# Optimization experiments

Measured on AMD Instinct MI355X. Metric: run time of the kernel, lower is better.

## Reference

```python
import jax, jax.numpy as jnp
import numpy as np

D_MODEL = 1024
H = 16
D_K = D_MODEL // H
B = 2
S = 2048


def setup_inputs() -> dict:
    key = jax.random.key(0)
    ks = jax.random.split(key, 11)
    scale = 1.0 / np.sqrt(D_MODEL)
    inp = {
        "query": jax.random.normal(ks[0], (B, S, D_MODEL), jnp.float32),
        "key_in": jax.random.normal(ks[1], (B, S, D_MODEL), jnp.float32),
        "value": jax.random.normal(ks[2], (B, S, D_MODEL), jnp.float32),
        # causal mask, broadcast over heads: 1 = keep, 0 = masked
        "mask": jnp.tril(jnp.ones((S, S), jnp.int32))[None, None, :, :].repeat(B, axis=0),
        "w_q": jax.random.normal(ks[3], (D_MODEL, D_MODEL), jnp.float32) * scale,
        "b_q": jax.random.normal(ks[4], (D_MODEL,), jnp.float32) * 0.01,
        "w_k": jax.random.normal(ks[5], (D_MODEL, D_MODEL), jnp.float32) * scale,
        "b_k": jax.random.normal(ks[6], (D_MODEL,), jnp.float32) * 0.01,
        "w_v": jax.random.normal(ks[7], (D_MODEL, D_MODEL), jnp.float32) * scale,
        "b_v": jax.random.normal(ks[8], (D_MODEL,), jnp.float32) * 0.01,
        "w_out": jax.random.normal(ks[9], (D_MODEL, D_MODEL), jnp.float32) * scale,
        "b_out": jax.random.normal(ks[10], (D_MODEL,), jnp.float32) * 0.01,
    }
    return inp


def _split_heads(x):
    # [B,S,D] -> [B,H,S,d_k]
    b, s, _ = x.shape
    return x.reshape(b, s, H, D_K).transpose(0, 2, 1, 3)


def reference(query, key_in, value, mask, w_q, b_q, w_k, b_k, w_v, b_v, w_out, b_out):
    q = _split_heads(query @ w_q.T + b_q)
    k = _split_heads(key_in @ w_k.T + b_k)
    v = _split_heads(value @ w_v.T + b_v)
    scores = jnp.einsum("bhqd,bhkd->bhqk", q, k) / jnp.sqrt(jnp.float32(D_K))
    scores = jnp.where(mask == 0, jnp.float32(-1e9), scores)
    attn = jax.nn.softmax(scores, axis=-1)  # dropout rate 0.0 -> identity
    out = jnp.einsum("bhqk,bhkd->bhqd", attn, v)
    out = out.transpose(0, 2, 1, 3).reshape(query.shape[0], -1, D_MODEL)
    return out @ w_out.T + b_out
```

## Files before the change

kernel.cpp:

```cpp
#include <hip/hip_runtime.h>
#include <hip/hip_bf16.h>

#define D_MODEL 1024
#define NH 16
#define DKH 64
#define BB 2
#define SS 2048
#define MTOT (BB * SS)

typedef __hip_bfloat16 bf16;
typedef __attribute__((ext_vector_type(8))) short short8;
typedef __attribute__((ext_vector_type(4))) short short4v;
typedef __attribute__((ext_vector_type(4))) float floatx4;

__device__ __forceinline__ bf16 f2bf(float x) { return __float2bfloat16(x); }

__device__ __forceinline__ void async_cp16(const void* g, void* l) {
  __builtin_amdgcn_global_load_lds(
      (const __attribute__((address_space(1))) unsigned int*)g,
      (__attribute__((address_space(3))) unsigned int*)l, 16, 0, 0);
}

__global__ __launch_bounds__(256) void convert_kernel(
    const float* __restrict__ wq, const float* __restrict__ wk,
    const float* __restrict__ wv, const float* __restrict__ wo,
    const float* __restrict__ qi, const float* __restrict__ ki,
    const float* __restrict__ vi, bf16* __restrict__ Wb,
    bf16* __restrict__ Qi, bf16* __restrict__ Ki, bf16* __restrict__ Vi) {
  const int id = blockIdx.x * 256 + threadIdx.x;
  const float* src;
  bf16* dst;
  if (id < (1 << 20)) {
    const int m = id >> 18, loc = id & 0x3FFFF;
    src = ((m == 0) ? wq : (m == 1) ? wk : (m == 2) ? wv : wo) + (size_t)loc * 4;
    dst = Wb + ((size_t)m << 20) + (size_t)loc * 4;
  } else {
    const int t = id - (1 << 20);
    const int m = t >> 20, loc = t & 0xFFFFF;
    src = ((m == 0) ? qi : (m == 1) ? ki : vi) + (size_t)loc * 4;
    dst = ((m == 0) ? Qi : (m == 1) ? Ki : Vi) + (size_t)loc * 4;
  }
  const float4 v = *(const float4*)src;
  short4v s;
  bf16* pb = (bf16*)&s;
  pb[0] = f2bf(v.x); pb[1] = f2bf(v.y); pb[2] = f2bf(v.z); pb[3] = f2bf(v.w);
  *(short4v*)dst = s;
}

__device__ __forceinline__ void gemm_qkv_body(const bf16* __restrict__ A,
                                              const bf16* __restrict__ W,
                                              const float* __restrict__ Bi,
                                              bf16* __restrict__ C, int mode) {
  constexpr int N = 1024, K = 1024;
  __shared__ bf16 As[2][128 * 32];
  __shared__ bf16 Ws[2][128 * 32];

  const int tid = threadIdx.x;
  const int w = tid >> 6, lane = tid & 63, quad = lane >> 4, n16 = lane & 15;
  const int bx = blockIdx.x;
  const int bm = bx & 31, bn = bx >> 5;
  const int wm = (w & 1) * 64, wn = (w >> 1) * 64;

  const int rb = lane >> 2, cb = lane & 3;

  const bf16* Ag0 = A + (size_t)(bm * 128) * K;
  const bf16* Wg0 = W + (size_t)(bn * 128) * K;

  auto issue = [&](int buf, int k0) {
#pragma unroll
    for (int ii = 0; ii < 2; ii++) {
      const int R = w * 32 + ii * 16 + rb;
      async_cp16(Ag0 + (size_t)R * K + k0 + cb * 8,
                 (void*)&As[buf][(w * 32 + ii * 16) * 32]);
      async_cp16(Wg0 + (size_t)R * K + k0 + cb * 8,
                 (void*)&Ws[buf][(w * 32 + ii * 16) * 32]);
    }
  };

  floatx4 acc[4][4] = {};
  issue(0, 0);
  int buf = 0;
  for (int k0 = 0; k0 < K; k0 += 32) {
    __syncthreads();
    if (k0 + 32 < K) issue(buf ^ 1, k0 + 32);

    short8 af[4], bfr[4];
#pragma unroll
    for (int i = 0; i < 4; i++)
      af[i] = *(const short8*)(&As[buf][(wm + i * 16 + n16) * 32 + quad * 8]);
#pragma unroll
    for (int j = 0; j < 4; j++)
      bfr[j] = *(const short8*)(&Ws[buf][(wn + j * 16 + n16) * 32 + quad * 8]);
#pragma unroll
    for (int i = 0; i < 4; i++)
#pragma unroll
      for (int j = 0; j < 4; j++)
        acc[i][j] = __builtin_amdgcn_mfma_f32_16x16x32_bf16(af[i], bfr[j], acc[i][j], 0, 0, 0);
    buf ^= 1;
  }

  float bv[4];
#pragma unroll
  for (int j = 0; j < 4; j++) bv[j] = Bi[bn * 128 + wn + j * 16 + n16];

#pragma unroll
  for (int i = 0; i < 4; i++) {
    const int rowb = bm * 128 + wm + i * 16 + quad * 4;
#pragma unroll
    for (int j = 0; j < 4; j++) {
      const int col = bn * 128 + wn + j * 16 + n16;
      if (mode == 1) {
        short4v s;
        bf16* pb = (bf16*)&s;
#pragma unroll
        for (int r = 0; r < 4; r++) pb[r] = f2bf(acc[i][j][r] + bv[j]);
        *(short4v*)(C + (size_t)col * MTOT + rowb) = s;
      } else {
#pragma unroll
        for (int r = 0; r < 4; r++)
          C[(size_t)(rowb + r) * N + col] = f2bf(acc[i][j][r] + bv[j]);
      }
    }
  }
}

__global__ __launch_bounds__(256) void gemm_qkv_kernel(
    const bf16* __restrict__ Qi, const bf16* __restrict__ Ki,
    const bf16* __restrict__ Vi, const bf16* __restrict__ Wb,
    const float* __restrict__ bq, const float* __restrict__ bk,
    const float* __restrict__ bv, bf16* __restrict__ Qw,
    bf16* __restrict__ Kw, bf16* __restrict__ VTw) {
  const int z = blockIdx.z;
  const bf16* A = (z == 0) ? Qi : (z == 1) ? Ki : Vi;
  const bf16* W = Wb + ((size_t)z << 20);
  const float* Bi = (z == 0) ? bq : (z == 1) ? bk : bv;
  bf16* C = (z == 0) ? Qw : (z == 1) ? Kw : VTw;
  gemm_qkv_body(A, W, Bi, C, (z == 2) ? 1 : 0);
}

__global__ __launch_bounds__(256) void gemm_out_kernel(
    const bf16* __restrict__ A, const bf16* __restrict__ W,
    const float* __restrict__ Bi, float* __restrict__ C) {
  constexpr int N = 1024, K = 1024;
  __shared__ bf16 As[2][64 * 32];
  __shared__ bf16 Ws[2][64 * 32];

  const int tid = threadIdx.x;
  const int w = tid >> 6, lane = tid & 63, quad = lane >> 4, n16 = lane & 15;
  const int bx = blockIdx.x;
  const int bm = bx & 63, bn = bx >> 6;
  const int wm = w * 16;

  const int rb = lane >> 2, cb = lane & 3;

  const bf16* Ag0 = A + (size_t)(bm * 64) * K;
  const bf16* Wg0 = W + (size_t)(bn * 64) * K;

  auto issue = [&](int buf, int kk) {
    const int R = w * 16 + rb;
    async_cp16(Ag0 + (size_t)R * K + kk + cb * 8, (void*)&As[buf][(w * 16) * 32]);
    async_cp16(Wg0 + (size_t)R * K + kk + cb * 8, (void*)&Ws[buf][(w * 16) * 32]);
  };

  floatx4 acc[4] = {};
  issue(0, 0);
  int buf = 0;
  for (int k0 = 0; k0 < K; k0 += 32) {
    __syncthreads();
    if (k0 + 32 < K) issue(buf ^ 1, k0 + 32);

    short8 af = *(const short8*)(&As[buf][(wm + n16) * 32 + quad * 8]);
#pragma unroll
    for (int j = 0; j < 4; j++) {
      short8 bfr = *(const short8*)(&Ws[buf][(j * 16 + n16) * 32 + quad * 8]);
      acc[j] = __builtin_amdgcn_mfma_f32_16x16x32_bf16(af, bfr, acc[j], 0, 0, 0);
    }
    buf ^= 1;
  }

  float bv[4];
#pragma unroll
  for (int j = 0; j < 4; j++) bv[j] = Bi[bn * 64 + j * 16 + n16];

  const int rowb = bm * 64 + wm + quad * 4;
#pragma unroll
  for (int j = 0; j < 4; j++) {
    const int col = bn * 64 + j * 16 + n16;
#pragma unroll
    for (int r = 0; r < 4; r++)
      C[(size_t)(rowb + r) * N + col] = acc[j][r] + bv[j];
  }
}

__global__ __launch_bounds__(256) void attn_kernel(const bf16* __restrict__ Q,
                                                   const bf16* __restrict__ Kg,
                                                   const bf16* __restrict__ VT,
                                                   bf16* __restrict__ O) {
  constexpr int BN = 128, LDK = 72, LDV = 136, LDP = 136;
  __shared__ bf16 Ks[128 * LDK];
  __shared__ bf16 Vs[64 * LDV];
  __shared__ bf16 Pw[4 * 16 * LDP];

  const int tid = threadIdx.x;
  const int w = tid >> 6, lane = tid & 63, quad = lane >> 4, n16 = lane & 15;
  const int hb = blockIdx.x;
  const int h = hb & 15, b = hb >> 4, p = blockIdx.y;
  const size_t qoff = (size_t)b * SS * D_MODEL + h * DKH;
  const bf16* VTh = VT + (size_t)(h * DKH) * MTOT + (size_t)b * SS;

  const int kvr = tid >> 3, ck = tid & 7;
  const int dd = tid >> 4, cv = tid & 15;

  short8 kreg[4], vreg[4];
  auto loadKV = [&](int kv0) {
#pragma unroll
    for (int ii = 0; ii < 4; ii++) {
      kreg[ii] = *(const short8*)(Kg + qoff + (size_t)(kv0 + ii * 32 + kvr) * D_MODEL + ck * 8);
      vreg[ii] = *(const short8*)(VTh + (size_t)(ii * 16 + dd) * MTOT + kv0 + cv * 8);
    }
  };

  for (int hf = 0; hf < 2; hf++) {
    const int q0 = (hf == 0) ? p * 64 : (31 - p) * 64;
    const int q0w = q0 + w * 16;
    const int nt = (q0 + 191) >> 7;

    short8 aQ0, aQ1;
    {
      const bf16* qp = Q + qoff + (size_t)(q0w + n16) * D_MODEL + quad * 8;
      aQ0 = *(const short8*)(qp);
      aQ1 = *(const short8*)(qp + 32);
    }

    floatx4 facc[4] = {};
    float l_p[4] = {0.f, 0.f, 0.f, 0.f};

    loadKV(0);
    for (int t = 0; t < nt; t++) {
#pragma unroll
      for (int ii = 0; ii < 4; ii++) {
        *(short8*)(&Ks[(ii * 32 + kvr) * LDK + ck * 8]) = kreg[ii];
        *(short8*)(&Vs[(ii * 16 + dd) * LDV + cv * 8]) = vreg[ii];
      }
      __syncthreads();
      if (t + 1 < nt) loadKV((t + 1) * BN);

      const int kv0 = t * BN;
      const bool lastT = (t == nt - 1);
      float pv[8][4];
      const int qrow_base = q0w + quad * 4;
#pragma unroll
      for (int blk = 0; blk < 8; blk++) {
        floatx4 z = {};
        short8 bk0 = *(const short8*)(&Ks[(blk * 16 + n16) * LDK + quad * 8]);
        short8 bk1 = *(const short8*)(&Ks[(blk * 16 + n16) * LDK + 32 + quad * 8]);
        z = __builtin_amdgcn_mfma_f32_16x16x32_bf16(aQ0, bk0, z, 0, 0, 0);
        z = __builtin_amdgcn_mfma_f32_16x16x32_bf16(aQ1, bk1, z, 0, 0, 0);
        if (lastT) {
          const int kvg = kv0 + blk * 16 + n16;
#pragma unroll
          for (int r = 0; r < 4; r++) {
            float pe = __expf(z[r] * 0.125f);
            if (kvg > qrow_base + r) pe = 0.f;
            pv[blk][r] = pe;
            l_p[r] += pe;
          }
        } else {
#pragma unroll
          for (int r = 0; r < 4; r++) {
            const float pe = __expf(z[r] * 0.125f);
            pv[blk][r] = pe;
            l_p[r] += pe;
          }
        }
      }

      bf16* pw = &Pw[w * 16 * LDP];
#pragma unroll
      for (int blk = 0; blk < 8; blk++)
#pragma unroll
        for (int r = 0; r < 4; r++)
          pw[(quad * 4 + r) * LDP + blk * 16 + n16] = f2bf(pv[blk][r]);

      short8 aP[4];
#pragma unroll
      for (int c = 0; c < 4; c++)
        aP[c] = *(const short8*)(&pw[n16 * LDP + c * 32 + quad * 8]);

#pragma unroll
      for (int d = 0; d < 4; d++)
#pragma unroll
        for (int c = 0; c < 4; c++) {
          short8 bvf = *(const short8*)(&Vs[(d * 16 + n16) * LDV + c * 32 + quad * 8]);
          facc[d] = __builtin_amdgcn_mfma_f32_16x16x32_bf16(aP[c], bvf, facc[d], 0, 0, 0);
        }
      __syncthreads();
    }

#pragma unroll
    for (int off = 1; off < 16; off <<= 1)
#pragma unroll
      for (int r = 0; r < 4; r++) l_p[r] += __shfl_xor(l_p[r], off, 64);

#pragma unroll
    for (int r = 0; r < 4; r++) {
      const float inv = 1.f / l_p[r];
      const int qrow = q0w + quad * 4 + r;
      bf16* op = O + qoff + (size_t)qrow * D_MODEL;
#pragma unroll
      for (int d = 0; d < 4; d++) op[d * 16 + n16] = f2bf(facc[d][r] * inv);
    }
  }
}

extern "C" void kernel_launch(void* const* d_in, const int* in_sizes, int n_in,
                              void* d_out, int out_size, void* d_ws, size_t ws_size,
                              hipStream_t stream) {
  (void)in_sizes; (void)n_in; (void)out_size; (void)ws_size;
  const float* query  = (const float*)d_in[0];
  const float* key_in = (const float*)d_in[1];
  const float* value  = (const float*)d_in[2];
  const float* w_q = (const float*)d_in[4];
  const float* b_q = (const float*)d_in[5];
  const float* w_k = (const float*)d_in[6];
  const float* b_k = (const float*)d_in[7];
  const float* w_v = (const float*)d_in[8];
  const float* b_v = (const float*)d_in[9];
  const float* w_o = (const float*)d_in[10];
  const float* b_o = (const float*)d_in[11];
  float* outp = (float*)d_out;

  const size_t mat = (size_t)MTOT * D_MODEL;
  bf16* Qws  = (bf16*)d_ws;
  bf16* Kws  = Qws + mat;
  bf16* VTws = Kws + mat;
  bf16* Wb   = VTws + mat;
  bf16* Vi   = Wb + 4 * (size_t)(1 << 20);
  bf16* Qi = (bf16*)d_out;
  bf16* Ki = Qi + mat;

  convert_kernel<<<16384, 256, 0, stream>>>(w_q, w_k, w_v, w_o, query, key_in,
                                            value, Wb, Qi, Ki, Vi);

  dim3 gq(256, 1, 3);
  gemm_qkv_kernel<<<gq, 256, 0, stream>>>(Qi, Ki, Vi, Wb, b_q, b_k, b_v, Qws,
                                          Kws, VTws);
  dim3 ga(NH * BB, 16);
  attn_kernel<<<ga, 256, 0, stream>>>(Qws, Kws, VTws, Qws);
  gemm_out_kernel<<<1024, 256, 0, stream>>>(Qws, Wb + ((size_t)3 << 20), b_o, outp);
}
```

Before: 241.5 us.

## Double-buffer attention K/V LDS tiles with XOR swizzle and transposed score MFMA

Double-buffers the K and V shared-memory tiles so the trailing __syncthreads per KV step is dropped, and prefetches the next half's first tile across the two query halves. Replaces padded LDS rows with an XOR swizzle to avoid bank conflicts. Swaps the MFMA operands so each lane holds four consecutive keys for one query, which lets P be written as packed 4-element vectors and shortens the row-sum reduction. Also raises MFMA priority with setprio and adds a two-waves-per-SIMD occupancy hint. LDS use goes up, which could limit occupancy.

```diff
diff --git a/kernel.cpp b/kernel.cpp
--- a/kernel.cpp
+++ b/kernel.cpp
@@ -192,14 +192,14 @@
   }
 }
 
-__global__ __launch_bounds__(256) void attn_kernel(const bf16* __restrict__ Q,
-                                                   const bf16* __restrict__ Kg,
-                                                   const bf16* __restrict__ VT,
-                                                   bf16* __restrict__ O) {
-  constexpr int BN = 128, LDK = 72, LDV = 136, LDP = 136;
-  __shared__ bf16 Ks[128 * LDK];
-  __shared__ bf16 Vs[64 * LDV];
-  __shared__ bf16 Pw[4 * 16 * LDP];
+__global__ __launch_bounds__(256, 2) void attn_kernel(const bf16* __restrict__ Q,
+                                                      const bf16* __restrict__ Kg,
+                                                      const bf16* __restrict__ VT,
+                                                      bf16* __restrict__ O) {
+  constexpr int BN = 128;
+  __shared__ bf16 Ks[2][128 * 64];
+  __shared__ bf16 Vs[2][64 * 128];
+  __shared__ bf16 Pw[4][16 * 128];
 
   const int tid = threadIdx.x;
   const int w = tid >> 6, lane = tid & 63, quad = lane >> 4, n16 = lane & 15;
@@ -210,6 +210,9 @@
 
   const int kvr = tid >> 3, ck = tid & 7;
   const int dd = tid >> 4, cv = tid & 15;
+  const int wk = (kvr & 7) << 3;
+  const int wv = (dd & 7) << 3;
+  const int swz = (n16 & 7) << 3;
 
   short8 kreg[4], vreg[4];
   auto loadKV = [&](int kv0) {
@@ -219,6 +222,10 @@
       vreg[ii] = *(const short8*)(VTh + (size_t)(ii * 16 + dd) * MTOT + kv0 + cv * 8);
     }
   };
+
+  bf16* pwb = &Pw[w][0];
+  loadKV(0);
+  int buf = 0;
 
   for (int hf = 0; hf < 2; hf++) {
     const int q0 = (hf == 0) ? p * 64 : (31 - p) * 64;
@@ -233,82 +240,79 @@
     }
 
     floatx4 facc[4] = {};
-    float l_p[4] = {0.f, 0.f, 0.f, 0.f};
-
-    loadKV(0);
+    float lsum = 0.f;
+
     for (int t = 0; t < nt; t++) {
 #pragma unroll
       for (int ii = 0; ii < 4; ii++) {
-        *(short8*)(&Ks[(ii * 32 + kvr) * LDK + ck * 8]) = kreg[ii];
-        *(short8*)(&Vs[(ii * 16 + dd) * LDV + cv * 8]) = vreg[ii];
+        *(short8*)(&Ks[buf][(ii * 32 + kvr) * 64 + ((ck * 8) ^ wk)]) = kreg[ii];
+        *(short8*)(&Vs[buf][(ii * 16 + dd) * 128 + ((cv * 8) ^ wv)]) = vreg[ii];
       }
+      if (t + 1 < nt) loadKV((t + 1) * BN);
+      else if (hf == 0) loadKV(0);
       __syncthreads();
-      if (t + 1 < nt) loadKV((t + 1) * BN);
 
       const int kv0 = t * BN;
       const bool lastT = (t == nt - 1);
-      float pv[8][4];
-      const int qrow_base = q0w + quad * 4;
+      const bf16* ksb = &Ks[buf][0];
+
 #pragma unroll
       for (int blk = 0; blk < 8; blk++) {
+        const int krow = blk * 16 + n16;
+        short8 ak0 = *(const short8*)(ksb + krow * 64 + ((quad * 8) ^ swz));
+        short8 ak1 = *(const short8*)(ksb + krow * 64 + ((quad * 8 + 32) ^ swz));
         floatx4 z = {};
-        short8 bk0 = *(const short8*)(&Ks[(blk * 16 + n16) * LDK + quad * 8]);
-        short8 bk1 = *(const short8*)(&Ks[(blk * 16 + n16) * LDK + 32 + quad * 8]);
-        z = __builtin_amdgcn_mfma_f32_16x16x32_bf16(aQ0, bk0, z, 0, 0, 0);
-        z = __builtin_amdgcn_mfma_f32_16x16x32_bf16(aQ1, bk1, z, 0, 0, 0);
+        z = __builtin_amdgcn_mfma_f32_16x16x32_bf16(ak0, aQ0, z, 0, 0, 0);
+        z = __builtin_amdgcn_mfma_f32_16x16x32_bf16(ak1, aQ1, z, 0, 0, 0);
+        short4v s;
+        bf16* pb = (bf16*)&s;
         if (lastT) {
-          const int kvg = kv0 + blk * 16 + n16;
+          const int kbase = kv0 + blk * 16 + quad * 4, qcol = q0w + n16;
 #pragma unroll
           for (int r = 0; r < 4; r++) {
             float pe = __expf(z[r] * 0.125f);
-            if (kvg > qrow_base + r) pe = 0.f;
-            pv[blk][r] = pe;
-            l_p[r] += pe;
+            if (kbase + r > qcol) pe = 0.f;
+            lsum += pe;
+            pb[r] = f2bf(pe);
           }
         } else {
 #pragma unroll
           for (int r = 0; r < 4; r++) {
             const float pe = __expf(z[r] * 0.125f);
-            pv[blk][r] = pe;
-            l_p[r] += pe;
+            lsum += pe;
+            pb[r] = f2bf(pe);
           }
         }
+        *(short4v*)(pwb + n16 * 128 + ((blk * 16 + quad * 4) ^ swz)) = s;
       }
 
-      bf16* pw = &Pw[w * 16 * LDP];
-#pragma unroll
-      for (int blk = 0; blk < 8; blk++)
-#pragma unroll
-        for (int r = 0; r < 4; r++)
-          pw[(quad * 4 + r) * LDP + blk * 16 + n16] = f2bf(pv[blk][r]);
-
       short8 aP[4];
 #pragma unroll
       for (int c = 0; c < 4; c++)
-        aP[c] = *(const short8*)(&pw[n16 * LDP + c * 32 + quad * 8]);
-
+        aP[c] = *(const short8*)(pwb + n16 * 128 + ((c * 32 + quad * 8) ^ swz));
+
+      const bf16* vsb = &Vs[buf][0];
+      __builtin_amdgcn_s_setprio(1);
 #pragma unroll
       for (int d = 0; d < 4; d++)
 #pragma unroll
         for (int c = 0; c < 4; c++) {
-          short8 bvf = *(const short8*)(&Vs[(d * 16 + n16) * LDV + c * 32 + quad * 8]);
+          short8 bvf = *(const short8*)(vsb + (d * 16 + n16) * 128 + ((c * 32 + quad * 8) ^ swz));
           facc[d] = __builtin_amdgcn_mfma_f32_16x16x32_bf16(aP[c], bvf, facc[d], 0, 0, 0);
         }
-      __syncthreads();
-    }
-
-#pragma unroll
-    for (int off = 1; off < 16; off <<= 1)
-#pragma unroll
-      for (int r = 0; r < 4; r++) l_p[r] += __shfl_xor(l_p[r], off, 64);
-
+      __builtin_amdgcn_s_setprio(0);
+      buf ^= 1;
+    }
+
+    lsum += __shfl_xor(lsum, 16);
+    lsum += __shfl_xor(lsum, 32);
 #pragma unroll
     for (int r = 0; r < 4; r++) {
-      const float inv = 1.f / l_p[r];
+      const float linv = 1.f / __shfl(lsum, quad * 4 + r);
       const int qrow = q0w + quad * 4 + r;
       bf16* op = O + qoff + (size_t)qrow * D_MODEL;
 #pragma unroll
-      for (int d = 0; d < 4; d++) op[d * 16 + n16] = f2bf(facc[d][r] * inv);
+      for (int d = 0; d < 4; d++) op[d * 16 + n16] = f2bf(facc[d][r] * linv);
     }
   }
 }
```

Result: faster. 233.1 us (-3.5%).
